# Optimization experiments

Hardware: AMD Instinct MI355X
Metric: run time of the kernel (lower is better)

Reference implementation:

```python
import jax, jax.numpy as jnp
import numpy as np

HEADS, HEAD_SIZE, FREQS, MAX_PERIOD = 16, 64, 256, 10000
D_MODEL = 1024
NEG_INF = -1e9


def sinusoid_embedding(seq_len, frequencies, max_period):
    # Interleaved sin/cos sinusoid table, shape (seq_len, frequencies).
    pos = np.arange(seq_len, dtype=np.float64)[:, None]
    idx = np.arange(frequencies)[None, :]
    inv_freq = max_period ** (-(idx // 2 * 2) / frequencies)
    angle = pos * inv_freq
    table = np.where(idx % 2 == 0, np.sin(angle), np.cos(angle))
    return table.astype(np.float32)


def relative_causal(scores):
    # scores: (b, n, q, v) with v indexing relative distance d = q - k.
    # Returns a[..., q, k] = scores[..., q, q - k] (k > q entries are masked later).
    L = scores.shape[-1]
    d = jnp.clip(jnp.arange(L)[:, None] - jnp.arange(L)[None, :], 0, L - 1)  # (q, k)
    return jnp.take_along_axis(scores, d[None, None, :, :], axis=-1)


def setup_inputs() -> dict:
    key = jax.random.key(0)
    ks = jax.random.split(key, 4)
    u = np.sqrt(3.0)
    inp = jax.random.normal(ks[0], (2, 2048, D_MODEL), dtype=jnp.float32)
    qkv = jax.random.uniform(ks[1], (D_MODEL, 3, HEADS, HEAD_SIZE), jnp.float32, -u, u)
    q_bias = jnp.zeros((HEADS, HEAD_SIZE), jnp.float32)
    positional = jax.random.uniform(ks[2], (FREQS, HEADS, HEAD_SIZE), jnp.float32, -u, u)
    out_kernel = jax.random.uniform(ks[3], (HEADS * HEAD_SIZE, D_MODEL), jnp.float32, -u, u)
    out_bias = jnp.zeros((D_MODEL,), jnp.float32)
    return {"input": inp, "qkv": qkv, "q_bias": q_bias, "positional": positional,
            "out_kernel": out_kernel, "out_bias": out_bias}


def reference(input, qkv, q_bias, positional, out_kernel, out_bias):
    b, s, x = input.shape
    n, h = HEADS, HEAD_SIZE
    # QKV projection with unit-scaling forward factor.
    w = qkv * (3.0 * x * h * n) ** -0.25
    q, k, v = jnp.einsum('bsx,xAnh->Abnsh', input, w)  # each (b, n, s, h)
    q = q + q_bias[:, None, :]
    # Content scores.
    a = jnp.einsum('bnqh,bnkh->bnqk', q, k) * h ** -0.5
    # Relative-positional scores (Transformer-XL style).
    sins = jnp.asarray(np.sqrt(2.0) * sinusoid_embedding(s, FREQS, MAX_PERIOD))
    emb = jnp.einsum('sf,fnh->nsh', sins, positional * FREQS ** -0.5)
    pos_scores = jnp.einsum('bnqh,nvh->bnqv', q, emb) * h ** -0.5
    a = a + relative_causal(pos_scores)
    # Causal mask + softmax.
    mask = jnp.tril(jnp.ones((s, s), dtype=bool))
    a = jax.nn.softmax(jnp.where(mask, a, NEG_INF), axis=-1)
    # Weighted sum and output projection (Dense, scale_for='both').
    o = jnp.einsum('bnqk,bnkh->bqnh', a, v).reshape(b, s, n * h)
    fan_in, fan_out = out_kernel.shape
    out = o @ (out_kernel * (fan_in * fan_out) ** -0.25) + out_bias
    return out
```

## Files before the change

kernel.cpp:

```cpp
#include <hip/hip_runtime.h>
#include <math.h>

#define BATCH 2
#define SEQ 2048
#define DMODEL 1024
#define HEADS 16
#define HSIZE 64
#define FREQS 256
#define NH 1024
#define QKVN 3072

typedef __bf16 bf16;
typedef __bf16 bf16x8 __attribute__((ext_vector_type(8)));
typedef float f32x4 __attribute__((ext_vector_type(4)));

static __device__ __forceinline__ unsigned short bf16_bits(float v) {
    bf16 b = (bf16)v; return __builtin_bit_cast(unsigned short, b);
}

static __device__ __forceinline__ void gload16(const void* g, void* l) {
    __builtin_amdgcn_global_load_lds(
        (const __attribute__((address_space(1))) unsigned int*)g,
        (__attribute__((address_space(3))) unsigned int*)l, 16, 0, 0);
}

__global__ __launch_bounds__(256) void prep_kernel(
    const float* __restrict__ inp, const float* __restrict__ qkv_w,
    const float* __restrict__ out_kernel, const float* __restrict__ positional,
    bf16* __restrict__ a_bf, bf16* __restrict__ wt_qkv,
    bf16* __restrict__ wt_out, bf16* __restrict__ wt_pos,
    bf16* __restrict__ sins_bf)
{
    __shared__ float tile[32][33];
    const int id = blockIdx.x, t = threadIdx.x;

    if (id < 4096) {
        int i = id * 256 + t;
        float4 v = ((const float4*)inp)[i];
        ushort4 o;
        o.x = bf16_bits(v.x); o.y = bf16_bits(v.y);
        o.z = bf16_bits(v.z); o.w = bf16_bits(v.w);
        ((ushort4*)a_bf)[i] = o;
        return;
    }
    if (id < 6144) {
        int i = (id - 4096) * 256 + t;
        int s = i >> 8, f = i & 255;
        double e = -(double)((f >> 1) << 1) / (double)FREQS;
        double invf = pow(10000.0, e);
        double ang = (double)s * invf;
        double v = (f & 1) ? cos(ang) : sin(ang);
        sins_bf[i] = (bf16)(float)(1.4142135623730951 * v);
        return;
    }
    int id2 = id - 6144;
    const float* src; bf16* dst; int R, C, c0, r0;
    if (id2 < 3072) {
        src = qkv_w; dst = wt_qkv; R = 1024; C = 3072;
        c0 = (id2 % 96) * 32; r0 = (id2 / 96) * 32;
    } else if (id2 < 4096) {
        id2 -= 3072;
        src = out_kernel; dst = wt_out; R = 1024; C = 1024;
        c0 = (id2 & 31) * 32; r0 = (id2 >> 5) * 32;
    } else {
        id2 -= 4096;
        src = positional; dst = wt_pos; R = 256; C = 1024;
        c0 = (id2 & 31) * 32; r0 = (id2 >> 5) * 32;
    }
    const int tx = t & 31, ty = t >> 5;
#pragma unroll
    for (int i = 0; i < 4; i++)
        tile[ty + i * 8][tx] = src[(size_t)(r0 + ty + i * 8) * C + c0 + tx];
    __syncthreads();
#pragma unroll
    for (int i = 0; i < 4; i++)
        dst[(size_t)(c0 + ty + i * 8) * R + r0 + tx] = (bf16)tile[tx][ty + i * 8];
}

template<int EPI>
__global__ __launch_bounds__(256) void mfma_gemm(
    const bf16* __restrict__ A, const bf16* __restrict__ Bt,
    int K, float alpha, const float* __restrict__ bias,
    float* __restrict__ outf, bf16* __restrict__ ob0, bf16* __restrict__ ob1,
    bf16* __restrict__ ob2,
    const bf16* __restrict__ A2, const bf16* __restrict__ Bt2,
    bf16* __restrict__ ob3, float alpha2)
{
    __shared__ __align__(16) bf16 Atile[2][128 * 32];
    __shared__ __align__(16) bf16 Btile[2][128 * 32];

    const int t    = threadIdx.x;
    const int lane = t & 63;
    const int w    = t >> 6;
    const int quad = lane >> 4;
    const int l16  = lane & 15;
    const int wm   = (w >> 1) * 64;
    const int wn   = (w & 1) * 64;

    bool embp = false;
    int m0 = blockIdx.y * 128, n0 = blockIdx.x * 128, Kl = K;
    const bf16* Ap = A; const bf16* Btp = Bt; float al = alpha;
    if constexpr (EPI == 1) {
        if (blockIdx.x >= 24) {
            if (blockIdx.y >= 16) return;
            embp = true;
            n0 = (blockIdx.x - 24) * 128;
            Kl = FREQS; Ap = A2; Btp = Bt2; al = alpha2;
        }
    }
    const bool swapv = (EPI == 1) && !embp && (n0 >= 2048);

    const int rS = t >> 2;
    const int cS = (t & 3) ^ ((rS >> 1) & 3);
    const bf16* ag0 = Ap  + (size_t)(m0 + rS) * Kl + cS * 8;
    const bf16* ag1 = ag0 + (size_t)64 * Kl;
    const bf16* bg0 = Btp + (size_t)(n0 + rS) * Kl + cS * 8;
    const bf16* bg1 = bg0 + (size_t)64 * Kl;

    int aoff[4], boff[4];
#pragma unroll
    for (int mi = 0; mi < 4; ++mi) {
        int r = wm + mi * 16 + l16;
        aoff[mi] = r * 32 + ((quad ^ ((r >> 1) & 3)) * 8);
    }
#pragma unroll
    for (int ni = 0; ni < 4; ++ni) {
        int r = wn + ni * 16 + l16;
        boff[ni] = r * 32 + ((quad ^ ((r >> 1) & 3)) * 8);
    }

    gload16(ag0, (char*)Atile[0] + t * 16);
    gload16(ag1, (char*)Atile[0] + 4096 + t * 16);
    gload16(bg0, (char*)Btile[0] + t * 16);
    gload16(bg1, (char*)Btile[0] + 4096 + t * 16);

    const int nK = Kl >> 5;
    f32x4 acc[4][4] = {};

    for (int kk = 0; kk < nK; ++kk) {
        __syncthreads();
        if (kk + 1 < nK) {
            ag0 += 32; ag1 += 32; bg0 += 32; bg1 += 32;
            char* ad = (char*)Atile[(kk + 1) & 1];
            char* bd = (char*)Btile[(kk + 1) & 1];
            gload16(ag0, ad + t * 16); gload16(ag1, ad + 4096 + t * 16);
            gload16(bg0, bd + t * 16); gload16(bg1, bd + 4096 + t * 16);
        }
        const bf16* ab = Atile[kk & 1];
        const bf16* bb = Btile[kk & 1];
        bf16x8 af[4], bfr[4];
#pragma unroll
        for (int mi = 0; mi < 4; ++mi) af[mi] = *(const bf16x8*)(ab + aoff[mi]);
#pragma unroll
        for (int ni = 0; ni < 4; ++ni) bfr[ni] = *(const bf16x8*)(bb + boff[ni]);

        if (!swapv) {
#pragma unroll
            for (int mi = 0; mi < 4; ++mi)
#pragma unroll
                for (int ni = 0; ni < 4; ++ni)
                    acc[mi][ni] = __builtin_amdgcn_mfma_f32_16x16x32_bf16(
                        af[mi], bfr[ni], acc[mi][ni], 0, 0, 0);
        } else {
#pragma unroll
            for (int mi = 0; mi < 4; ++mi)
#pragma unroll
                for (int ni = 0; ni < 4; ++ni)
                    acc[mi][ni] = __builtin_amdgcn_mfma_f32_16x16x32_bf16(
                        bfr[ni], af[mi], acc[mi][ni], 0, 0, 0);
        }
    }

    if constexpr (EPI == 0) {
#pragma unroll
        for (int mi = 0; mi < 4; ++mi)
#pragma unroll
            for (int ni = 0; ni < 4; ++ni) {
                int col = n0 + wn + ni * 16 + l16;
                float bb = bias[col];
#pragma unroll
                for (int rg = 0; rg < 4; ++rg) {
                    int row = m0 + wm + mi * 16 + quad * 4 + rg;
                    outf[(size_t)row * NH + col] = acc[mi][ni][rg] * al + bb;
                }
            }
    } else {
        if (embp) {
#pragma unroll
            for (int mi = 0; mi < 4; ++mi)
#pragma unroll
                for (int ni = 0; ni < 4; ++ni) {
                    int col = n0 + wn + ni * 16 + l16;
                    int head = col >> 6, h = col & 63;
#pragma unroll
                    for (int rg = 0; rg < 4; ++rg) {
                        int d = m0 + wm + mi * 16 + quad * 4 + rg;
                        int hs = h ^ (((d + 63) & 7) << 3);
                        ob3[((size_t)(head * SEQ + d)) * 64 + hs] =
                            (bf16)(acc[mi][ni][rg] * al);
                    }
                }
        } else if (n0 >= 2048) {
#pragma unroll
            for (int mi = 0; mi < 4; ++mi)
#pragma unroll
                for (int ni = 0; ni < 4; ++ni) {
                    int mcol = m0 + wm + mi * 16 + l16;
                    int bb = mcol >> 11, s = mcol & 2047;
#pragma unroll
                    for (int rg = 0; rg < 4; ++rg) {
                        int hg = n0 + wn + ni * 16 + quad * 4 + rg;
                        int head = (hg & 1023) >> 6, h = hg & 63;
                        int ss = s ^ ((h & 7) << 3);
                        ob2[((size_t)((bb * 16 + head) * 64 + h)) * SEQ + ss] =
                            (bf16)(acc[mi][ni][rg] * al);
                    }
                }
        } else {
            const int whichk = (n0 >= 1024);
#pragma unroll
            for (int mi = 0; mi < 4; ++mi)
#pragma unroll
                for (int ni = 0; ni < 4; ++ni) {
                    int cg   = (n0 + wn + ni * 16 + l16) & 1023;
                    int head = cg >> 6, h = cg & 63;
                    float qbv = whichk ? 0.0f : bias[cg];
#pragma unroll
                    for (int rg = 0; rg < 4; ++rg) {
                        int row = m0 + wm + mi * 16 + quad * 4 + rg;
                        int bb = row >> 11, s = row & 2047;
                        float v = acc[mi][ni][rg] * al;
                        if (whichk) {
                            int hs = h ^ ((s & 7) << 3);
                            ob1[((size_t)((bb * 16 + head) * SEQ + s)) * 64 + hs] = (bf16)v;
                        } else {
                            ob0[((size_t)((bb * 16 + head) * SEQ + s)) * 64 + h] =
                                (bf16)((v + qbv) * 0.125f);
                        }
                    }
                }
        }
    }
}

__global__ __launch_bounds__(256, 2) void attn_kernel(
    const bf16* __restrict__ Qb, const bf16* __restrict__ Kb,
    const bf16* __restrict__ Vtb, const bf16* __restrict__ Eb,
    bf16* __restrict__ o)
{
    __shared__ __align__(16) bf16 Ks[2][4096];
    __shared__ __align__(16) bf16 Vts[2][4096];
    __shared__ __align__(16) bf16 Es[256 * 64];
    __shared__ __align__(16) bf16 PS[4][16][72];

    const int t    = threadIdx.x;
    const int lane = t & 63;
    const int w    = t >> 6;
    const int quad = lane >> 4;
    const int l16  = lane & 15;

    const int bx = blockIdx.x;
    const int b  = bx >> 4, n = bx & 15;
    const int yy = blockIdx.y;
    const int qc = (yy < 8) ? (15 - 2 * yy) : (2 * yy - 16);
    const int q0 = qc * 128;
    const int KT = 2 * qc + 2;
    const int qw0 = q0 + 16 * w;
    const int qw1 = qw0 + 64;

    const bf16* __restrict__ Qp = Qb  + (size_t)bx * SEQ * 64;
    const bf16* __restrict__ Kp = Kb  + (size_t)bx * SEQ * 64;
    const bf16* __restrict__ Vp = Vtb + (size_t)bx * SEQ * 64;
    const bf16* __restrict__ Ep = Eb  + (size_t)n  * SEQ * 64;

    const int key8 = (l16 & 7) << 3;
    const int ec0  = ((quad * 8) ^ key8) * 2;
    const int ec1  = ((32 + quad * 8) ^ key8) * 2;

    bf16x8 qf[2][2];
    qf[0][0] = *(const bf16x8*)(Qp + (size_t)(qw0 + l16) * 64 + quad * 8);
    qf[0][1] = *(const bf16x8*)(Qp + (size_t)(qw0 + l16) * 64 + 32 + quad * 8);
    qf[1][0] = *(const bf16x8*)(Qp + (size_t)(qw1 + l16) * 64 + quad * 8);
    qf[1][1] = *(const bf16x8*)(Qp + (size_t)(qw1 + l16) * 64 + 32 + quad * 8);

    int dsta[4];
    bool condp[4];
#pragma unroll
    for (int rg = 0; rg < 4; ++rg) {
        int rr   = quad * 4 + rg;
        int l16c = (rr + 15 - l16) & 15;
        dsta[rg]  = ((lane & 48) + l16c) << 2;
        condp[rg] = rr > l16c;
    }

    f32x4 O[2][4] = {};
    float lsum[2][4] = {};

    {
        gload16(Kp + t * 8,        (char*)Ks[0] + t * 16);
        gload16(Kp + 2048 + t * 8, (char*)Ks[0] + 4096 + t * 16);
        gload16(Vp + (size_t)(t >> 3) * SEQ + (t & 7) * 8,        (char*)Vts[0] + t * 16);
        gload16(Vp + (size_t)((t >> 3) + 32) * SEQ + (t & 7) * 8, (char*)Vts[0] + 4096 + t * 16);
        const long D0 = (long)q0 - 63;
#pragma unroll
        for (int g = 0; g < 6; ++g)
            gload16(Ep + (D0 + 32 * g) * 64 + t * 8, (char*)Es + g * 4096 + t * 16);
    }

    for (int kt = 0; kt < KT; ++kt) {
        const int k0 = kt * 64;
        __syncthreads();

        const int nt = kt + 1;
        if (nt < KT) {
            bf16* kd = Ks[nt & 1];
            bf16* vd = Vts[nt & 1];
            const bf16* ksrc = Kp + nt * 4096;
            gload16(ksrc + t * 8,        (char*)kd + t * 16);
            gload16(ksrc + 2048 + t * 8, (char*)kd + 4096 + t * 16);
            gload16(Vp + (size_t)(t >> 3) * SEQ + nt * 64 + (t & 7) * 8,
                    (char*)vd + t * 16);
            gload16(Vp + (size_t)((t >> 3) + 32) * SEQ + nt * 64 + (t & 7) * 8,
                    (char*)vd + 4096 + t * 16);
            const long d0 = (long)q0 - nt * 64 - 63;
            const int rI = (-64 * nt) & 255;
            gload16(Ep + d0 * 64 + t * 8,        (char*)Es + rI * 128 + t * 16);
            gload16(Ep + (d0 + 32) * 64 + t * 8, (char*)Es + rI * 128 + 4096 + t * 16);
        }

        const char* kb = (const char*)Ks[kt & 1];
        const char* vb = (const char*)Vts[kt & 1];
        bf16x8 kf[4][2], vf[4][2];
#pragma unroll
        for (int j = 0; j < 4; ++j) {
            const char* kp = kb + (j * 16 + l16) * 128;
            kf[j][0] = *(const bf16x8*)(kp + ec0);
            kf[j][1] = *(const bf16x8*)(kp + ec1);
            const char* vp = vb + (j * 16 + l16) * 128;
            vf[j][0] = *(const bf16x8*)(vp + ec0);
            vf[j][1] = *(const bf16x8*)(vp + ec1);
        }

        const bool last = (nt == KT);
#pragma unroll
        for (int c = 0; c < 2; ++c) {
            if (c == 0 && last) continue;
            const int qwc = c ? qw1 : qw0;

            f32x4 pa[5];
            const int rb = 16 * w + 64 * c - k0;
#pragma unroll
            for (int jj = 0; jj < 5; ++jj) {
                const char* ep = (const char*)Es + ((rb + 16 * jj + l16) & 255) * 128;
                bf16x8 e0 = *(const bf16x8*)(ep + ec0);
                bf16x8 e1 = *(const bf16x8*)(ep + ec1);
                f32x4 a = {0, 0, 0, 0};
                a = __builtin_amdgcn_mfma_f32_16x16x32_bf16(qf[c][1], e1, a, 0, 0, 0);
                a = __builtin_amdgcn_mfma_f32_16x16x32_bf16(qf[c][0], e0, a, 0, 0, 0);
                pa[jj] = a;
            }

            f32x4 S[4];
#pragma unroll
            for (int j = 0; j < 4; ++j) {
                f32x4 a = {0, 0, 0, 0};
                a = __builtin_amdgcn_mfma_f32_16x16x32_bf16(qf[c][1], kf[j][1], a, 0, 0, 0);
                a = __builtin_amdgcn_mfma_f32_16x16x32_bf16(qf[c][0], kf[j][0], a, 0, 0, 0);
                S[j] = a;
            }

#pragma unroll
            for (int j = 0; j < 4; ++j) {
#pragma unroll
                for (int rg = 0; rg < 4; ++rg) {
                    float vsel = condp[rg] ? pa[4 - j][rg] : pa[3 - j][rg];
                    int pv = __builtin_amdgcn_ds_permute(dsta[rg], __float_as_int(vsel));
                    float sv = S[j][rg] + __int_as_float(pv);
                    bool valid = (k0 + j * 16 + l16) <= (qwc + quad * 4 + rg);
                    S[j][rg] = valid ? __expf(sv) : 0.0f;
                }
            }
#pragma unroll
            for (int rg = 0; rg < 4; ++rg)
                lsum[c][rg] += S[0][rg] + S[1][rg] + S[2][rg] + S[3][rg];

#pragma unroll
            for (int j = 0; j < 4; ++j)
#pragma unroll
                for (int rg = 0; rg < 4; ++rg)
                    PS[w][quad * 4 + rg][j * 16 + l16] = (bf16)S[j][rg];
            bf16x8 pf0 = *(const bf16x8*)(&PS[w][l16][quad * 8]);
            bf16x8 pf1 = *(const bf16x8*)(&PS[w][l16][32 + quad * 8]);

#pragma unroll
            for (int j4 = 0; j4 < 4; ++j4) {
                O[c][j4] = __builtin_amdgcn_mfma_f32_16x16x32_bf16(pf1, vf[j4][1], O[c][j4], 0, 0, 0);
                O[c][j4] = __builtin_amdgcn_mfma_f32_16x16x32_bf16(pf0, vf[j4][0], O[c][j4], 0, 0, 0);
            }
        }
    }

#pragma unroll
    for (int c = 0; c < 2; ++c) {
#pragma unroll
        for (int rg = 0; rg < 4; ++rg) {
            float s = lsum[c][rg];
            s += __shfl_xor(s, 1);
            s += __shfl_xor(s, 2);
            s += __shfl_xor(s, 4);
            s += __shfl_xor(s, 8);
            float inv = 1.0f / s;
            int q = (c ? qw1 : qw0) + quad * 4 + rg;
            size_t ro = ((size_t)(b * SEQ + q)) * NH + n * 64;
            o[ro +  0 + l16] = (bf16)(O[c][0][rg] * inv);
            o[ro + 16 + l16] = (bf16)(O[c][1][rg] * inv);
            o[ro + 32 + l16] = (bf16)(O[c][2][rg] * inv);
            o[ro + 48 + l16] = (bf16)(O[c][3][rg] * inv);
        }
    }
}

extern "C" void kernel_launch(void* const* d_in, const int* in_sizes, int n_in,
                              void* d_out, int out_size, void* d_ws, size_t ws_size,
                              hipStream_t stream) {
    const float* inp        = (const float*)d_in[0];
    const float* qkv_w      = (const float*)d_in[1];
    const float* q_bias     = (const float*)d_in[2];
    const float* positional = (const float*)d_in[3];
    const float* out_kernel = (const float*)d_in[4];
    const float* out_bias   = (const float*)d_in[5];

    char* p = (char*)d_ws;
    auto alloc = [&](size_t bytes) {
        char* q = p; p += (bytes + 255) & ~(size_t)255; return q;
    };
    bf16* qbuf    = (bf16*)alloc((size_t)BATCH * HEADS * SEQ * HSIZE * 2);
    bf16* kbuf    = (bf16*)alloc((size_t)BATCH * HEADS * SEQ * HSIZE * 2);
    bf16* vtbuf   = (bf16*)alloc((size_t)BATCH * HEADS * SEQ * HSIZE * 2);
    bf16* embT    = (bf16*)alloc((size_t)HEADS * SEQ * HSIZE * 2);
    bf16* sins_bf = (bf16*)alloc((size_t)SEQ * FREQS * 2);
    bf16* obuf    = (bf16*)alloc((size_t)BATCH * SEQ * NH * 2);
    bf16* a_bf    = (bf16*)alloc((size_t)BATCH * SEQ * DMODEL * 2);
    bf16* wt_qkv  = (bf16*)alloc((size_t)QKVN * DMODEL * 2);
    bf16* wt_out  = (bf16*)alloc((size_t)NH * DMODEL * 2);
    bf16* wt_pos  = (bf16*)alloc((size_t)NH * FREQS * 2);

    const float qkv_scale = (float)pow(3.0 * DMODEL * HSIZE * HEADS, -0.25);
    const float emb_scale = 0.0625f;
    const float out_scale = 0.03125f;

    prep_kernel<<<10496, 256, 0, stream>>>(
        inp, qkv_w, out_kernel, positional, a_bf, wt_qkv, wt_out, wt_pos, sins_bf);

    mfma_gemm<1><<<dim3(32, 32), 256, 0, stream>>>(
        a_bf, wt_qkv, DMODEL, qkv_scale, q_bias, nullptr, qbuf, kbuf, vtbuf,
        sins_bf, wt_pos, embT, emb_scale);

    attn_kernel<<<dim3(32, 16), 256, 0, stream>>>(
        qbuf, kbuf, vtbuf, embT, obuf);

    mfma_gemm<0><<<dim3(8, 32), 256, 0, stream>>>(
        obuf, wt_out, DMODEL, out_scale, out_bias, (float*)d_out,
        nullptr, nullptr, nullptr, nullptr, nullptr, nullptr, 0.0f);
}
```

Before: 263.6 us.

## Split long causal attention rows across two blocks, read positional table from global

Query chunks 8-15 are now split into two halves along the key range. Each half writes unnormalized partial outputs and row sums to a workspace, and a new combine kernel adds the halves and normalizes them. This balances the triangular causal workload over 24 block rows instead of 16. The positional embedding tile is dropped from LDS and read directly from global memory, which frees LDS so occupancy can rise to 3 blocks per SM. Other changes: log2(e) is folded into the Q scale so exp2f replaces __expf, the sinusoid table is computed with range-reduced float sin/cos in fewer blocks, and the extra kernel launch and fp32 partial traffic are the cost.

```diff
diff --git a/kernel.cpp b/kernel.cpp
--- a/kernel.cpp
+++ b/kernel.cpp
@@ -13,6 +13,9 @@
 typedef __bf16 bf16;
 typedef __bf16 bf16x8 __attribute__((ext_vector_type(8)));
 typedef float f32x4 __attribute__((ext_vector_type(4)));
+
+__constant__ int c_qc[24] = {15,15,7,14,14,13,13,6,12,12,5,11,11,10,10,4,9,9,8,8,3,2,1,0};
+__constant__ int c_hh[24] = { 0, 1,0, 0, 1, 0, 1,0, 0, 1,0, 0, 1, 0, 1,0,0,1,0,1,0,0,0,0};
 
 static __device__ __forceinline__ unsigned short bf16_bits(float v) {
     bf16 b = (bf16)v; return __builtin_bit_cast(unsigned short, b);
@@ -43,17 +46,24 @@
         ((ushort4*)a_bf)[i] = o;
         return;
     }
-    if (id < 6144) {
-        int i = (id - 4096) * 256 + t;
-        int s = i >> 8, f = i & 255;
+    if (id < 4128) {
+        const int br = id - 4096;
+        const int f = t;
         double e = -(double)((f >> 1) << 1) / (double)FREQS;
         double invf = pow(10000.0, e);
-        double ang = (double)s * invf;
-        double v = (f & 1) ? cos(ang) : sin(ang);
-        sins_bf[i] = (bf16)(float)(1.4142135623730951 * v);
+        const double twopi = 6.283185307179586;
+        const double inv2pi = 0.15915494309189535;
+        for (int j = 0; j < 64; ++j) {
+            int s = br * 64 + j;
+            double ang = (double)s * invf;
+            double r = ang - floor(ang * inv2pi) * twopi;
+            float rf = (float)r;
+            float v = (f & 1) ? cosf(rf) : sinf(rf);
+            sins_bf[s * 256 + f] = (bf16)(1.41421356f * v);
+        }
         return;
     }
-    int id2 = id - 6144;
+    int id2 = id - 4128;
     const float* src; bf16* dst; int R, C, c0, r0;
     if (id2 < 3072) {
         src = qkv_w; dst = wt_qkv; R = 1024; C = 3072;
@@ -195,8 +205,7 @@
 #pragma unroll
                     for (int rg = 0; rg < 4; ++rg) {
                         int d = m0 + wm + mi * 16 + quad * 4 + rg;
-                        int hs = h ^ (((d + 63) & 7) << 3);
-                        ob3[((size_t)(head * SEQ + d)) * 64 + hs] =
+                        ob3[((size_t)(head * SEQ + d)) * 64 + h] =
                             (bf16)(acc[mi][ni][rg] * al);
                     }
                 }
@@ -235,7 +244,7 @@
                             ob1[((size_t)((bb * 16 + head) * SEQ + s)) * 64 + hs] = (bf16)v;
                         } else {
                             ob0[((size_t)((bb * 16 + head) * SEQ + s)) * 64 + h] =
-                                (bf16)((v + qbv) * 0.125f);
+                                (bf16)((v + qbv) * 0.18033688f);
                         }
                     }
                 }
@@ -243,14 +252,13 @@
     }
 }
 
-__global__ __launch_bounds__(256, 2) void attn_kernel(
+__global__ __launch_bounds__(256, 3) void attn_kernel(
     const bf16* __restrict__ Qb, const bf16* __restrict__ Kb,
     const bf16* __restrict__ Vtb, const bf16* __restrict__ Eb,
-    bf16* __restrict__ o)
+    bf16* __restrict__ o, float* __restrict__ pO, float* __restrict__ pl)
 {
     __shared__ __align__(16) bf16 Ks[2][4096];
     __shared__ __align__(16) bf16 Vts[2][4096];
-    __shared__ __align__(16) bf16 Es[256 * 64];
     __shared__ __align__(16) bf16 PS[4][16][72];
 
     const int t    = threadIdx.x;
@@ -261,10 +269,12 @@
 
     const int bx = blockIdx.x;
     const int b  = bx >> 4, n = bx & 15;
-    const int yy = blockIdx.y;
-    const int qc = (yy < 8) ? (15 - 2 * yy) : (2 * yy - 16);
+    const int qc = c_qc[blockIdx.y];
+    const int hh = c_hh[blockIdx.y];
+    const bool split = qc >= 8;
+    const int ks = hh ? qc + 1 : 0;
+    const int ke = split ? (hh ? 2 * qc + 2 : qc + 1) : 2 * qc + 2;
     const int q0 = qc * 128;
-    const int KT = 2 * qc + 2;
     const int qw0 = q0 + 16 * w;
     const int qw1 = qw0 + 64;
 
@@ -297,35 +307,28 @@
     float lsum[2][4] = {};
 
     {
-        gload16(Kp + t * 8,        (char*)Ks[0] + t * 16);
-        gload16(Kp + 2048 + t * 8, (char*)Ks[0] + 4096 + t * 16);
-        gload16(Vp + (size_t)(t >> 3) * SEQ + (t & 7) * 8,        (char*)Vts[0] + t * 16);
-        gload16(Vp + (size_t)((t >> 3) + 32) * SEQ + (t & 7) * 8, (char*)Vts[0] + 4096 + t * 16);
-        const long D0 = (long)q0 - 63;
-#pragma unroll
-        for (int g = 0; g < 6; ++g)
-            gload16(Ep + (D0 + 32 * g) * 64 + t * 8, (char*)Es + g * 4096 + t * 16);
-    }
-
-    for (int kt = 0; kt < KT; ++kt) {
+        char* kd = (char*)Ks[ks & 1];
+        char* vd = (char*)Vts[ks & 1];
+        const bf16* ksrc = Kp + ks * 4096;
+        gload16(ksrc + t * 8,        kd + t * 16);
+        gload16(ksrc + 2048 + t * 8, kd + 4096 + t * 16);
+        gload16(Vp + (size_t)(t >> 3) * SEQ + ks * 64 + (t & 7) * 8,        vd + t * 16);
+        gload16(Vp + (size_t)((t >> 3) + 32) * SEQ + ks * 64 + (t & 7) * 8, vd + 4096 + t * 16);
+    }
+
+    for (int kt = ks; kt < ke; ++kt) {
         const int k0 = kt * 64;
         __syncthreads();
 
         const int nt = kt + 1;
-        if (nt < KT) {
-            bf16* kd = Ks[nt & 1];
-            bf16* vd = Vts[nt & 1];
+        if (nt < ke) {
+            char* kd = (char*)Ks[nt & 1];
+            char* vd = (char*)Vts[nt & 1];
             const bf16* ksrc = Kp + nt * 4096;
-            gload16(ksrc + t * 8,        (char*)kd + t * 16);
-            gload16(ksrc + 2048 + t * 8, (char*)kd + 4096 + t * 16);
-            gload16(Vp + (size_t)(t >> 3) * SEQ + nt * 64 + (t & 7) * 8,
-                    (char*)vd + t * 16);
-            gload16(Vp + (size_t)((t >> 3) + 32) * SEQ + nt * 64 + (t & 7) * 8,
-                    (char*)vd + 4096 + t * 16);
-            const long d0 = (long)q0 - nt * 64 - 63;
-            const int rI = (-64 * nt) & 255;
-            gload16(Ep + d0 * 64 + t * 8,        (char*)Es + rI * 128 + t * 16);
-            gload16(Ep + (d0 + 32) * 64 + t * 8, (char*)Es + rI * 128 + 4096 + t * 16);
+            gload16(ksrc + t * 8,        kd + t * 16);
+            gload16(ksrc + 2048 + t * 8, kd + 4096 + t * 16);
+            gload16(Vp + (size_t)(t >> 3) * SEQ + nt * 64 + (t & 7) * 8,        vd + t * 16);
+            gload16(Vp + (size_t)((t >> 3) + 32) * SEQ + nt * 64 + (t & 7) * 8, vd + 4096 + t * 16);
         }
 
         const char* kb = (const char*)Ks[kt & 1];
@@ -341,19 +344,17 @@
             vf[j][1] = *(const bf16x8*)(vp + ec1);
         }
 
-        const bool last = (nt == KT);
 #pragma unroll
         for (int c = 0; c < 2; ++c) {
-            if (c == 0 && last) continue;
+            if (c == 0 && k0 >= q0 + 64) continue;
             const int qwc = c ? qw1 : qw0;
 
+            const bf16* eb = Ep + (ptrdiff_t)((qwc - k0 - 63 + l16) * 64) + quad * 8;
             f32x4 pa[5];
-            const int rb = 16 * w + 64 * c - k0;
 #pragma unroll
             for (int jj = 0; jj < 5; ++jj) {
-                const char* ep = (const char*)Es + ((rb + 16 * jj + l16) & 255) * 128;
-                bf16x8 e0 = *(const bf16x8*)(ep + ec0);
-                bf16x8 e1 = *(const bf16x8*)(ep + ec1);
+                bf16x8 e0 = *(const bf16x8*)(eb + jj * 1024);
+                bf16x8 e1 = *(const bf16x8*)(eb + jj * 1024 + 32);
                 f32x4 a = {0, 0, 0, 0};
                 a = __builtin_amdgcn_mfma_f32_16x16x32_bf16(qf[c][1], e1, a, 0, 0, 0);
                 a = __builtin_amdgcn_mfma_f32_16x16x32_bf16(qf[c][0], e0, a, 0, 0, 0);
@@ -377,7 +378,7 @@
                     int pv = __builtin_amdgcn_ds_permute(dsta[rg], __float_as_int(vsel));
                     float sv = S[j][rg] + __int_as_float(pv);
                     bool valid = (k0 + j * 16 + l16) <= (qwc + quad * 4 + rg);
-                    S[j][rg] = valid ? __expf(sv) : 0.0f;
+                    S[j][rg] = valid ? exp2f(sv) : 0.0f;
                 }
             }
 #pragma unroll
@@ -400,24 +401,68 @@
         }
     }
 
-#pragma unroll
-    for (int c = 0; c < 2; ++c) {
-#pragma unroll
-        for (int rg = 0; rg < 4; ++rg) {
-            float s = lsum[c][rg];
-            s += __shfl_xor(s, 1);
-            s += __shfl_xor(s, 2);
-            s += __shfl_xor(s, 4);
-            s += __shfl_xor(s, 8);
-            float inv = 1.0f / s;
-            int q = (c ? qw1 : qw0) + quad * 4 + rg;
-            size_t ro = ((size_t)(b * SEQ + q)) * NH + n * 64;
-            o[ro +  0 + l16] = (bf16)(O[c][0][rg] * inv);
-            o[ro + 16 + l16] = (bf16)(O[c][1][rg] * inv);
-            o[ro + 32 + l16] = (bf16)(O[c][2][rg] * inv);
-            o[ro + 48 + l16] = (bf16)(O[c][3][rg] * inv);
-        }
-    }
+    if (!split) {
+#pragma unroll
+        for (int c = 0; c < 2; ++c) {
+#pragma unroll
+            for (int rg = 0; rg < 4; ++rg) {
+                float s = lsum[c][rg];
+                s += __shfl_xor(s, 1);
+                s += __shfl_xor(s, 2);
+                s += __shfl_xor(s, 4);
+                s += __shfl_xor(s, 8);
+                float inv = 1.0f / s;
+                int q = (c ? qw1 : qw0) + quad * 4 + rg;
+                size_t ro = ((size_t)(b * SEQ + q)) * NH + n * 64;
+                o[ro +  0 + l16] = (bf16)(O[c][0][rg] * inv);
+                o[ro + 16 + l16] = (bf16)(O[c][1][rg] * inv);
+                o[ro + 32 + l16] = (bf16)(O[c][2][rg] * inv);
+                o[ro + 48 + l16] = (bf16)(O[c][3][rg] * inv);
+            }
+        }
+    } else {
+        const size_t pbase = (((size_t)(hh * 2 + b) * 16 + n) * 1024 + (size_t)(qc - 8) * 128);
+#pragma unroll
+        for (int c = 0; c < 2; ++c) {
+#pragma unroll
+            for (int rg = 0; rg < 4; ++rg) {
+                float s = lsum[c][rg];
+                s += __shfl_xor(s, 1);
+                s += __shfl_xor(s, 2);
+                s += __shfl_xor(s, 4);
+                s += __shfl_xor(s, 8);
+                int rloc = 16 * w + 64 * c + quad * 4 + rg;
+                if (l16 == 0) pl[pbase + rloc] = s;
+                float* po = pO + (pbase + rloc) * 64;
+                po[ 0 + l16] = O[c][0][rg];
+                po[16 + l16] = O[c][1][rg];
+                po[32 + l16] = O[c][2][rg];
+                po[48 + l16] = O[c][3][rg];
+            }
+        }
+    }
+}
+
+__global__ __launch_bounds__(256) void combine_kernel(
+    const float* __restrict__ pO, const float* __restrict__ pl,
+    bf16* __restrict__ o)
+{
+    const int e = blockIdx.x * 1024 + threadIdx.x * 4;
+    const int col = e & 63;
+    const int r   = (e >> 6) & 1023;
+    const int n   = (e >> 16) & 15;
+    const int b   = e >> 20;
+    const size_t i0 = (size_t)(b * 16 + n) * 1024 + r;
+    float4 va = *(const float4*)(pO + i0 * 64 + col);
+    float4 vb = *(const float4*)(pO + (size_t)2097152 + i0 * 64 + col);
+    float inv = 1.0f / (pl[i0] + pl[32768 + i0]);
+    ushort4 ov;
+    ov.x = bf16_bits((va.x + vb.x) * inv);
+    ov.y = bf16_bits((va.y + vb.y) * inv);
+    ov.z = bf16_bits((va.z + vb.z) * inv);
+    ov.w = bf16_bits((va.w + vb.w) * inv);
+    *(ushort4*)((unsigned short*)o +
+                ((size_t)(b * SEQ + 1024 + r)) * NH + n * 64 + col) = ov;
 }
 
 extern "C" void kernel_launch(void* const* d_in, const int* in_sizes, int n_in,
@@ -444,20 +489,24 @@
     bf16* wt_qkv  = (bf16*)alloc((size_t)QKVN * DMODEL * 2);
     bf16* wt_out  = (bf16*)alloc((size_t)NH * DMODEL * 2);
     bf16* wt_pos  = (bf16*)alloc((size_t)NH * FREQS * 2);
+    float* pO     = (float*)alloc((size_t)2 * 2 * 16 * 1024 * 64 * 4);
+    float* pl     = (float*)alloc((size_t)2 * 2 * 16 * 1024 * 4);
 
     const float qkv_scale = (float)pow(3.0 * DMODEL * HSIZE * HEADS, -0.25);
     const float emb_scale = 0.0625f;
     const float out_scale = 0.03125f;
 
-    prep_kernel<<<10496, 256, 0, stream>>>(
+    prep_kernel<<<8480, 256, 0, stream>>>(
         inp, qkv_w, out_kernel, positional, a_bf, wt_qkv, wt_out, wt_pos, sins_bf);
 
     mfma_gemm<1><<<dim3(32, 32), 256, 0, stream>>>(
         a_bf, wt_qkv, DMODEL, qkv_scale, q_bias, nullptr, qbuf, kbuf, vtbuf,
         sins_bf, wt_pos, embT, emb_scale);
 
-    attn_kernel<<<dim3(32, 16), 256, 0, stream>>>(
-        qbuf, kbuf, vtbuf, embT, obuf);
+    attn_kernel<<<dim3(32, 24), 256, 0, stream>>>(
+        qbuf, kbuf, vtbuf, embT, obuf, pO, pl);
+
+    combine_kernel<<<2048, 256, 0, stream>>>(pO, pl, obuf);
 
     mfma_gemm<0><<<dim3(8, 32), 256, 0, stream>>>(
         obuf, wt_out, DMODEL, out_scale, out_bias, (float*)d_out,
```

New measurement: 392.0 us. 1.49x slower.
